# Kernel tuning notes

Measured on AMD Instinct MI355X. Metric: run time of the kernel, lower is better.

## Reference

```python
import jax, jax.numpy as jnp
import numpy as np

B, S, CIN, COUT, W, M, P = 32, 8192, 2, 1, 64, 16, 24


def setup_inputs() -> dict:
    key = jax.random.key(0)
    ks = jax.random.split(key, 12)

    def lin(k, o, i):
        return (jax.random.uniform(k, (o, i), jnp.float32) * 2 - 1) / np.float32(np.sqrt(i))

    scale = np.float32(1.0 / (W * W))  # SpectralConv1d init scale 1/(in*out)
    return {
        "x": jax.random.normal(ks[0], (B, S, CIN), jnp.float32),
        "fc0_w": lin(ks[1], W, CIN),
        "fc0_b": jnp.zeros((W,), jnp.float32),
        "conv_wr": jax.random.uniform(ks[2], (4, W, W, M), jnp.float32) * scale,
        "conv_wi": jax.random.uniform(ks[3], (4, W, W, M), jnp.float32) * scale,
        "pw_w": lin(ks[4], 4 * W, W).reshape(4, W, W),  # 1x1 conv weights (out,in)
        "pw_b": jnp.zeros((4, W), jnp.float32),
        "fc1_w": lin(ks[5], 128, W),
        "fc1_b": jnp.zeros((128,), jnp.float32),
        "fc2_w": lin(ks[6], COUT, 128),
        "ica_w": lin(ks[7], P, 128),
        "ica_b": jnp.zeros((P,), jnp.float32),
    }


def spectral_conv(h, wr, wi, n):
    # h: (B, W, S). Keep first M rfft modes, complex-multiply, inverse rfft.
    xf = jnp.fft.rfft(h, axis=-1)[..., :M]          # (B, W, M) complex
    w = wr + 1j * wi                                 # (W, W, M)
    of = jnp.einsum('bix,iox->box', xf, w)           # (B, W, M)
    of = jnp.pad(of, ((0, 0), (0, 0), (0, n // 2 + 1 - M)))
    return jnp.fft.irfft(of, n=n, axis=-1)


def reference(x, fc0_w, fc0_b, conv_wr, conv_wi, pw_w, pw_b, fc1_w, fc1_b, fc2_w, ica_w, ica_b):
    b, s, _ = x.shape
    h = x @ fc0_w.T + fc0_b                          # lift: (B, S, W)
    h = h.transpose(0, 2, 1)                         # (B, W, S)
    for l in range(4):
        x1 = spectral_conv(h, conv_wr[l], conv_wi[l], s)
        x2 = jnp.einsum('oi,bis->bos', pw_w[l], h) + pw_b[l][None, :, None]
        h = x1 + x2
        if l < 3:                                    # no relu after layer 3 (as in torch code)
            h = jax.nn.relu(h)
    h = h.transpose(0, 2, 1)                         # (B, S, W)
    h = h @ fc1_w.T + fc1_b                          # (B, S, 128)
    h_ = jax.nn.relu(h)
    # broadcast ICA decomposition: (B,S,1,128)*(1,1,COUT,128)
    components = h_[:, :, None, :] * fc2_w[None, None, :, :]
    tc = components @ ica_w.T + ica_b                # (B, S, COUT, P)
    out = tc.sum(-1)                                 # (B, S, COUT)
    return out, tc
```

## Files before the change

kernel.cpp:

```cpp
#include <hip/hip_runtime.h>
#include <math.h>

#define SB 8192
#define NB 32
#define WC 64
#define NM 16
#define NKC 32
#define NP 24
#define NSC 16
#define LP 132


__global__ __launch_bounds__(256) void k_table(float* __restrict__ T) {
    int s = blockIdx.x * 256 + threadIdx.x;
    float* row = T + (size_t)s * NKC;
    #pragma unroll
    for (int k = 0; k < NM; ++k) {
        int m = (k * s) & (SB - 1);
        double ang = (double)m * (6.283185307179586476925286766559 / (double)SB);
        row[2 * k]     = (float)cos(ang);
        row[2 * k + 1] = (float)sin(ang);
    }
}

__global__ __launch_bounds__(256) void k_prep(const float* __restrict__ ica_w,
                                              const float* __restrict__ fc2_w,
                                              float* __restrict__ icaT) {
    int tid = blockIdx.x * 256 + threadIdx.x;
    int c = tid / NP;
    int p = tid - c * NP;
    icaT[c * NP + p] = ica_w[p * 128 + c] * fc2_w[c];
}

__global__ __launch_bounds__(256) void k_prepw(const float* __restrict__ pw_w,
                                               float* __restrict__ pwT) {
    int tid = blockIdx.x * 256 + threadIdx.x;
    int l = tid >> 12, k = (tid >> 6) & 63, o = tid & 63;
    pwT[tid] = pw_w[(size_t)l * 4096 + o * 64 + k];
}

__global__ __launch_bounds__(256) void k_lift(const float* __restrict__ x,
                                              const float* __restrict__ fc0_w,
                                              const float* __restrict__ fc0_b,
                                              float* __restrict__ h) {
    int b = blockIdx.y;
    int s = blockIdx.x * 256 + threadIdx.x;
    float2 xv = ((const float2*)x)[(size_t)b * SB + s];
    #pragma unroll
    for (int w = 0; w < WC; ++w) {
        float v = fmaf(xv.x, fc0_w[2 * w], fmaf(xv.y, fc0_w[2 * w + 1], fc0_b[w]));
        h[((size_t)(b * WC + w)) * SB + s] = v;
    }
}

__global__ __launch_bounds__(256) void k_dft(const float* __restrict__ h,
                                             const float* __restrict__ T,
                                             float* __restrict__ xfp) {
    __shared__ float u[12800];
    int blk = blockIdx.x;
    int b  = blk >> 4;
    int sc = blk & (NSC - 1);
    int t  = threadIdx.x;
    int lane = t & 63;
    int wv = __builtin_amdgcn_readfirstlane(t >> 6);
    int g  = lane >> 3;
    int j8 = lane & 7;

    float acc[8][4];
    #pragma unroll
    for (int i = 0; i < 8; ++i)
        #pragma unroll
        for (int m = 0; m < 4; ++m) acc[i][m] = 0.f;

    int ch_s = t >> 2, part = t & 3;
    const float* hb = h + ((size_t)(b * WC + ch_s)) * SB;

    for (int st = 0; st < 4; ++st) {
        int s_base = sc * 512 + st * 128;

        const float* hrow = hb + s_base;
        #pragma unroll
        for (int r = 0; r < 8; ++r) {
            int so = (part + 4 * r) * 4;
            float4 v = *(const float4*)(hrow + so);
            u[(so + 0) * 68 + ch_s] = v.x;
            u[(so + 1) * 68 + ch_s] = v.y;
            u[(so + 2) * 68 + ch_s] = v.z;
            u[(so + 3) * 68 + ch_s] = v.w;
        }
        {
            const float4* tsrc = (const float4*)(T + (size_t)s_base * NKC);
            float4* tdst = (float4*)(u + 8704);
            #pragma unroll
            for (int r = 0; r < 4; ++r) tdst[t + r * 256] = tsrc[t + r * 256];
        }
        __syncthreads();

        #pragma unroll 4
        for (int ss = 0; ss < 32; ++ss) {
            int s = wv * 32 + ss;
            float4 tv = *(const float4*)&u[8704 + s * 32 + j8 * 4];
            float4 h0 = *(const float4*)&u[s * 68 + g * 8];
            float4 h1 = *(const float4*)&u[s * 68 + g * 8 + 4];
            float hh[8] = {h0.x, h0.y, h0.z, h0.w, h1.x, h1.y, h1.z, h1.w};
            #pragma unroll
            for (int i = 0; i < 8; ++i) {
                acc[i][0] = fmaf(hh[i], tv.x, acc[i][0]);
                acc[i][1] = fmaf(hh[i], tv.y, acc[i][1]);
                acc[i][2] = fmaf(hh[i], tv.z, acc[i][2]);
                acc[i][3] = fmaf(hh[i], tv.w, acc[i][3]);
            }
        }
        __syncthreads();
    }

    {
        float* slot = u + (wv * 64 + lane) * 33;
        #pragma unroll
        for (int i = 0; i < 8; ++i)
            #pragma unroll
            for (int m = 0; m < 4; ++m) slot[i * 4 + m] = acc[i][m];
    }
    __syncthreads();

    float* dst = xfp + ((size_t)(sc * NB + b)) * 2048;
    float res[8];
    #pragma unroll
    for (int e = 0; e < 8; ++e) {
        int idx = t * 8 + e;
        int ch = idx >> 5, mode = idx & 31;
        int g2 = ch >> 3, i2 = ch & 7;
        int q2 = mode >> 2, m2 = mode & 3;
        int lane2 = g2 * 8 + q2;
        int v2 = i2 * 4 + m2;
        res[e] = u[lane2 * 33 + v2] + u[(64 + lane2) * 33 + v2]
               + u[(128 + lane2) * 33 + v2] + u[(192 + lane2) * 33 + v2];
    }
    float4* d4 = (float4*)(dst + t * 8);
    d4[0] = make_float4(res[0], res[1], res[2], res[3]);
    d4[1] = make_float4(res[4], res[5], res[6], res[7]);
}

__global__ __launch_bounds__(256) void k_red(const float* __restrict__ xfp,
                                             float* __restrict__ xf, int nsc) {
    int idx = blockIdx.x * 256 + threadIdx.x;
    int b = idx >> 11;
    int r = idx & 2047;
    float s = 0.f;
    #pragma unroll 8
    for (int sc = 0; sc < nsc; ++sc)
        s += xfp[((size_t)(sc * NB + b)) * 2048 + r];
    xf[idx] = s;
}

__global__ __launch_bounds__(256) void k_mix(const float* __restrict__ xf,
                                             const float* __restrict__ wr,
                                             const float* __restrict__ wi,
                                             float* __restrict__ ofT) {
    int tid = blockIdx.x * 256 + threadIdx.x;
    int k = tid & 15;
    int o = (tid >> 4) & 63;
    int b = tid >> 10;
    float orr = 0.f, oii = 0.f;
    const float2* xfb = (const float2*)(xf + (size_t)b * WC * NKC);
    #pragma unroll 4
    for (int i = 0; i < WC; ++i) {
        float2 cs = xfb[i * NM + k];
        float wrv = wr[(i * WC + o) * NM + k];
        float wiv = wi[(i * WC + o) * NM + k];
        orr = fmaf(cs.x, wrv, fmaf(cs.y, wiv, orr));
        oii = fmaf(cs.x, wiv, fmaf(-cs.y, wrv, oii));
    }
    float alpha = (k == 0 ? 1.f : 2.f) / (float)SB;
    ofT[((size_t)b * NKC + 2 * k) * 64 + o]     = alpha * orr;
    ofT[((size_t)b * NKC + 2 * k + 1) * 64 + o] = -alpha * oii;
}

__global__ __launch_bounds__(256) void k_update(float* __restrict__ h,
                                                const float* __restrict__ T,
                                                const float* __restrict__ ofT,
                                                const float* __restrict__ pwT,
                                                const float* __restrict__ pwb,
                                                int relu, float* __restrict__ xfp,
                                                int dodft) {
    __shared__ float u[96 * LP];
    float (*hS)[LP] = (float(*)[LP])u;
    int t = threadIdx.x;
    int b = blockIdx.y;
    int s0 = blockIdx.x * 128;
    int lane_s = t & 63;
    int g4 = __builtin_amdgcn_readfirstlane((t >> 6) & 3);
    int ob = g4 * 16;

    {
        int ch = t >> 2, part = t & 3;
        const float* hrow = h + ((size_t)(b * WC + ch)) * SB + s0;
        #pragma unroll
        for (int r = 0; r < 8; ++r) {
            int so = (part + 4 * r) * 4;
            *(float4*)&hS[ch][so] = *(const float4*)(hrow + so);
        }
    }
    {
        int sl = t >> 1, jj0 = (t & 1) * 16;
        const float4* src = (const float4*)(T + (size_t)(s0 + sl) * NKC + jj0);
        float4 a = src[0], c4 = src[1], d = src[2], e = src[3];
        hS[64 + jj0 +  0][sl] = a.x;  hS[64 + jj0 +  1][sl] = a.y;
        hS[64 + jj0 +  2][sl] = a.z;  hS[64 + jj0 +  3][sl] = a.w;
        hS[64 + jj0 +  4][sl] = c4.x; hS[64 + jj0 +  5][sl] = c4.y;
        hS[64 + jj0 +  6][sl] = c4.z; hS[64 + jj0 +  7][sl] = c4.w;
        hS[64 + jj0 +  8][sl] = d.x;  hS[64 + jj0 +  9][sl] = d.y;
        hS[64 + jj0 + 10][sl] = d.z;  hS[64 + jj0 + 11][sl] = d.w;
        hS[64 + jj0 + 12][sl] = e.x;  hS[64 + jj0 + 13][sl] = e.y;
        hS[64 + jj0 + 14][sl] = e.z;  hS[64 + jj0 + 15][sl] = e.w;
    }
    __syncthreads();

    float acc0[16], acc1[16];
    #pragma unroll
    for (int o = 0; o < 16; ++o) { acc0[o] = pwb[ob + o]; acc1[o] = pwb[ob + o]; }

    const float* wbase0 = pwT + ob;
    const float* wbase1 = ofT + ((size_t)b * NKC) * 64 + ob;

    for (int kc = 0; kc < 8; ++kc) {
        #pragma unroll
        for (int uu = 0; uu < 8; ++uu) {
            int k = kc * 8 + uu;
            float h0 = hS[k][lane_s];
            float h1 = hS[k][64 + lane_s];
            const float* w = wbase0 + k * 64;
            #pragma unroll
            for (int o = 0; o < 16; ++o) {
                acc0[o] = fmaf(w[o], h0, acc0[o]);
                acc1[o] = fmaf(w[o], h1, acc1[o]);
            }
        }
    }
    for (int kc = 0; kc < 4; ++kc) {
        #pragma unroll
        for (int uu = 0; uu < 8; ++uu) {
            int j = kc * 8 + uu;
            float h0 = hS[64 + j][lane_s];
            float h1 = hS[64 + j][64 + lane_s];
            const float* w = wbase1 + j * 64;
            #pragma unroll
            for (int o = 0; o < 16; ++o) {
                acc0[o] = fmaf(w[o], h0, acc0[o]);
                acc1[o] = fmaf(w[o], h1, acc1[o]);
            }
        }
    }

    if (relu) {
        #pragma unroll
        for (int o = 0; o < 16; ++o) {
            acc0[o] = fmaxf(acc0[o], 0.f);
            acc1[o] = fmaxf(acc1[o], 0.f);
        }
    }

    float* hw0 = h + (size_t)b * WC * SB + s0 + lane_s;
    float* hw1 = hw0 + 64;
    #pragma unroll
    for (int o = 0; o < 16; ++o) {
        hw0[(size_t)(ob + o) * SB] = acc0[o];
        hw1[(size_t)(ob + o) * SB] = acc1[o];
    }

    if (!dodft) return;

    __syncthreads();
    #pragma unroll
    for (int o = 0; o < 16; ++o) {
        u[lane_s * 65 + ob + o]        = acc0[o];
        u[(64 + lane_s) * 65 + ob + o] = acc1[o];
    }
    __syncthreads();

    int lane = t & 63;
    int wv = __builtin_amdgcn_readfirstlane(t >> 6);
    int g  = lane >> 3;
    int j8 = lane & 7;

    float dacc[8][4];
    #pragma unroll
    for (int i = 0; i < 8; ++i)
        #pragma unroll
        for (int m = 0; m < 4; ++m) dacc[i][m] = 0.f;

    #pragma unroll 4
    for (int ss = 0; ss < 32; ++ss) {
        int s = wv * 32 + ss;
        float tv0 = u[64 * LP + (j8 * 4 + 0) * LP + s];
        float tv1 = u[64 * LP + (j8 * 4 + 1) * LP + s];
        float tv2 = u[64 * LP + (j8 * 4 + 2) * LP + s];
        float tv3 = u[64 * LP + (j8 * 4 + 3) * LP + s];
        float4 h0 = *(const float4*)&u[s * 65 + g * 8];
        float4 h1 = *(const float4*)&u[s * 65 + g * 8 + 4];
        float hh[8] = {h0.x, h0.y, h0.z, h0.w, h1.x, h1.y, h1.z, h1.w};
        #pragma unroll
        for (int i = 0; i < 8; ++i) {
            dacc[i][0] = fmaf(hh[i], tv0, dacc[i][0]);
            dacc[i][1] = fmaf(hh[i], tv1, dacc[i][1]);
            dacc[i][2] = fmaf(hh[i], tv2, dacc[i][2]);
            dacc[i][3] = fmaf(hh[i], tv3, dacc[i][3]);
        }
    }

    __syncthreads();
    {
        float* slot = u + (wv * 64 + lane) * 33;
        #pragma unroll
        for (int i = 0; i < 8; ++i)
            #pragma unroll
            for (int m = 0; m < 4; ++m) slot[i * 4 + m] = dacc[i][m];
    }
    __syncthreads();

    float* dst = xfp + ((size_t)(blockIdx.x * NB + b)) * 2048;
    float res[8];
    #pragma unroll
    for (int e = 0; e < 8; ++e) {
        int idx = t * 8 + e;
        int ch = idx >> 5, mode = idx & 31;
        int g2 = ch >> 3, i2 = ch & 7;
        int q2 = mode >> 2, m2 = mode & 3;
        int lane2 = g2 * 8 + q2;
        int v2 = i2 * 4 + m2;
        res[e] = u[lane2 * 33 + v2] + u[(64 + lane2) * 33 + v2]
               + u[(128 + lane2) * 33 + v2] + u[(192 + lane2) * 33 + v2];
    }
    float4* d4 = (float4*)(dst + t * 8);
    d4[0] = make_float4(res[0], res[1], res[2], res[3]);
    d4[1] = make_float4(res[4], res[5], res[6], res[7]);
}

__global__ __launch_bounds__(256) void k_final(const float* __restrict__ h,
                                               const float* __restrict__ fc1_w,
                                               const float* __restrict__ fc1_b,
                                               const float* __restrict__ icaT,
                                               const float* __restrict__ ica_b,
                                               float* __restrict__ out,
                                               float* __restrict__ tc) {
    __shared__ float u_lds[6400];
    float (*hS)[68] = (float(*)[68])u_lds;
    int t = threadIdx.x;
    int b = blockIdx.y;
    int s0 = blockIdx.x * 64;
    int lane_s = t & 63;
    int wv = __builtin_amdgcn_readfirstlane(t >> 6);
    int c0 = wv * 32;

    {
        int sl = t & 63, chg = t >> 6;
        const float* hb = h + (size_t)b * WC * SB + s0 + sl;
        #pragma unroll
        for (int cc = 0; cc < 16; ++cc) {
            int ch = chg * 16 + cc;
            hS[sl][ch] = hb[(size_t)ch * SB];
        }
    }
    __syncthreads();

    float acc[NP];
    #pragma unroll
    for (int p = 0; p < NP; ++p) acc[p] = 0.f;

    for (int cq = 0; cq < 8; ++cq) {
        int c = c0 + 4 * cq;
        float tv0 = fc1_b[c], tv1 = fc1_b[c + 1], tv2 = fc1_b[c + 2], tv3 = fc1_b[c + 3];
        const float* w0 = fc1_w + (size_t)c * WC;
        const float* w1 = w0 + WC;
        const float* w2 = w1 + WC;
        const float* w3 = w2 + WC;
        for (int ioct = 0; ioct < 8; ++ioct) {
            float4 xa = *(const float4*)&hS[lane_s][ioct * 8];
            float4 xb = *(const float4*)&hS[lane_s][ioct * 8 + 4];
            float xs[8] = {xa.x, xa.y, xa.z, xa.w, xb.x, xb.y, xb.z, xb.w};
            #pragma unroll
            for (int uu = 0; uu < 8; ++uu) {
                int i = ioct * 8 + uu;
                tv0 = fmaf(w0[i], xs[uu], tv0);
                tv1 = fmaf(w1[i], xs[uu], tv1);
                tv2 = fmaf(w2[i], xs[uu], tv2);
                tv3 = fmaf(w3[i], xs[uu], tv3);
            }
        }
        tv0 = fmaxf(tv0, 0.f); tv1 = fmaxf(tv1, 0.f);
        tv2 = fmaxf(tv2, 0.f); tv3 = fmaxf(tv3, 0.f);
        const float* e0 = icaT + (size_t)c * NP;
        const float* e1 = e0 + NP;
        const float* e2 = e1 + NP;
        const float* e3 = e2 + NP;
        #pragma unroll
        for (int p = 0; p < NP; ++p)
            acc[p] = fmaf(tv0, e0[p], fmaf(tv1, e1[p],
                     fmaf(tv2, e2[p], fmaf(tv3, e3[p], acc[p]))));
    }

    __syncthreads();
    {
        float* slot = u_lds + ((t >> 6) * 64 + lane_s) * 25;
        #pragma unroll
        for (int p = 0; p < NP; ++p) slot[p] = acc[p];
    }
    __syncthreads();

    float* tcb = tc + ((size_t)b * SB + s0) * NP;
    #pragma unroll
    for (int r = 0; r < 6; ++r) {
        int e = t + r * 256;
        int s = e / NP, p = e - s * NP;
        float v = u_lds[s * 25 + p] + u_lds[(64 + s) * 25 + p]
                + u_lds[(128 + s) * 25 + p] + u_lds[(192 + s) * 25 + p]
                + ica_b[p];
        tcb[e] = v;
        u_lds[s * 25 + p] = v;
    }
    __syncthreads();
    if (t < 64) {
        float osum = 0.f;
        #pragma unroll
        for (int p = 0; p < NP; ++p) osum += u_lds[t * 25 + p];
        out[(size_t)b * SB + s0 + t] = osum;
    }
}

extern "C" void kernel_launch(void* const* d_in, const int* in_sizes, int n_in,
                              void* d_out, int out_size, void* d_ws, size_t ws_size,
                              hipStream_t stream) {
    const float* x     = (const float*)d_in[0];
    const float* fc0_w = (const float*)d_in[1];
    const float* fc0_b = (const float*)d_in[2];
    const float* cwr   = (const float*)d_in[3];
    const float* cwi   = (const float*)d_in[4];
    const float* pw_w  = (const float*)d_in[5];
    const float* pw_b  = (const float*)d_in[6];
    const float* fc1_w = (const float*)d_in[7];
    const float* fc1_b = (const float*)d_in[8];
    const float* fc2_w = (const float*)d_in[9];
    const float* ica_w = (const float*)d_in[10];
    const float* ica_b = (const float*)d_in[11];

    float* out = (float*)d_out;
    float* tc  = out + (size_t)NB * SB;

    float* ws   = (float*)d_ws;
    float* h    = ws;
    float* T    = ws + 16777216;
    float* xf   = ws + 17039360;
    float* ofT  = ws + 17104896;
    float* icaT = ws + 17170432;
    float* pwT  = ws + 17173504;
    float* xfp  = tc;

    k_table<<<32, 256, 0, stream>>>(T);
    k_prep<<<12, 256, 0, stream>>>(ica_w, fc2_w, icaT);
    k_prepw<<<64, 256, 0, stream>>>(pw_w, pwT);
    k_lift<<<dim3(32, 32), 256, 0, stream>>>(x, fc0_w, fc0_b, h);

    for (int l = 0; l < 4; ++l) {
        if (l == 0) {
            k_dft<<<NB * NSC, 256, 0, stream>>>(h, T, xfp);
            k_red<<<256, 256, 0, stream>>>(xfp, xf, NSC);
        } else {
            k_red<<<256, 256, 0, stream>>>(xfp, xf, 64);
        }
        k_mix<<<128, 256, 0, stream>>>(xf, cwr + (size_t)l * WC * WC * NM,
                                       cwi + (size_t)l * WC * WC * NM, ofT);
        k_update<<<dim3(64, 32), 256, 0, stream>>>(h, T, ofT,
                                                   pwT + (size_t)l * 4096,
                                                   pw_b + (size_t)l * WC,
                                                   (l < 3) ? 1 : 0,
                                                   xfp, (l < 3) ? 1 : 0);
    }

    k_final<<<dim3(128, 32), 256, 0, stream>>>(h, fc1_w, fc1_b, icaT, ica_b, out, tc);
}
```

Measured before the change: 425.8 us.

## Fuse layer-0 truncated DFT into the lift kernel

The lift kernel now keeps each 128-sample tile of lifted activations in shared memory and computes the partial 16-mode DFT directly, writing per-chunk partials in the same 64-chunk format the later layers use. This removes the separate k_dft launch and its re-read of the full h tensor from global memory. The layer-0 reduction now sums 64 partials instead of 16, and the lift kernel carries more shared memory and register pressure.

```diff
diff --git a/kernel.cpp b/kernel.cpp
--- a/kernel.cpp
+++ b/kernel.cpp
@@ -7,7 +7,6 @@
 #define NM 16
 #define NKC 32
 #define NP 24
-#define NSC 16
 #define LP 132
 
 
@@ -42,88 +41,82 @@
 __global__ __launch_bounds__(256) void k_lift(const float* __restrict__ x,
                                               const float* __restrict__ fc0_w,
                                               const float* __restrict__ fc0_b,
-                                              float* __restrict__ h) {
+                                              float* __restrict__ h,
+                                              const float* __restrict__ T,
+                                              float* __restrict__ xfp) {
+    __shared__ float u[12544];
+    int t = threadIdx.x;
     int b = blockIdx.y;
-    int s = blockIdx.x * 256 + threadIdx.x;
-    float2 xv = ((const float2*)x)[(size_t)b * SB + s];
-    #pragma unroll
-    for (int w = 0; w < WC; ++w) {
-        float v = fmaf(xv.x, fc0_w[2 * w], fmaf(xv.y, fc0_w[2 * w + 1], fc0_b[w]));
-        h[((size_t)(b * WC + w)) * SB + s] = v;
-    }
-}
-
-__global__ __launch_bounds__(256) void k_dft(const float* __restrict__ h,
-                                             const float* __restrict__ T,
-                                             float* __restrict__ xfp) {
-    __shared__ float u[12800];
-    int blk = blockIdx.x;
-    int b  = blk >> 4;
-    int sc = blk & (NSC - 1);
-    int t  = threadIdx.x;
+    int s0 = blockIdx.x * 128;
+    int sl = t & 127, half = t >> 7;
+    int cb = half * 32;
+
+    float2 xv = ((const float2*)x)[(size_t)b * SB + s0 + sl];
+    float* hcol = h + (size_t)b * WC * SB + s0 + sl;
+    #pragma unroll
+    for (int c = 0; c < 32; ++c) {
+        int ch = cb + c;
+        float v = fmaf(xv.x, fc0_w[2 * ch], fmaf(xv.y, fc0_w[2 * ch + 1], fc0_b[ch]));
+        hcol[(size_t)ch * SB] = v;
+        u[sl * 65 + ch] = v;
+    }
+    {
+        int sl2 = t >> 1, jj0 = (t & 1) * 16;
+        const float4* src = (const float4*)(T + (size_t)(s0 + sl2) * NKC + jj0);
+        float4 a = src[0], c4 = src[1], d = src[2], e = src[3];
+        float* Tt = u + 8320;
+        Tt[(jj0 +  0) * LP + sl2] = a.x;  Tt[(jj0 +  1) * LP + sl2] = a.y;
+        Tt[(jj0 +  2) * LP + sl2] = a.z;  Tt[(jj0 +  3) * LP + sl2] = a.w;
+        Tt[(jj0 +  4) * LP + sl2] = c4.x; Tt[(jj0 +  5) * LP + sl2] = c4.y;
+        Tt[(jj0 +  6) * LP + sl2] = c4.z; Tt[(jj0 +  7) * LP + sl2] = c4.w;
+        Tt[(jj0 +  8) * LP + sl2] = d.x;  Tt[(jj0 +  9) * LP + sl2] = d.y;
+        Tt[(jj0 + 10) * LP + sl2] = d.z;  Tt[(jj0 + 11) * LP + sl2] = d.w;
+        Tt[(jj0 + 12) * LP + sl2] = e.x;  Tt[(jj0 + 13) * LP + sl2] = e.y;
+        Tt[(jj0 + 14) * LP + sl2] = e.z;  Tt[(jj0 + 15) * LP + sl2] = e.w;
+    }
+    __syncthreads();
+
     int lane = t & 63;
     int wv = __builtin_amdgcn_readfirstlane(t >> 6);
     int g  = lane >> 3;
     int j8 = lane & 7;
 
-    float acc[8][4];
+    float dacc[8][4];
     #pragma unroll
     for (int i = 0; i < 8; ++i)
         #pragma unroll
-        for (int m = 0; m < 4; ++m) acc[i][m] = 0.f;
-
-    int ch_s = t >> 2, part = t & 3;
-    const float* hb = h + ((size_t)(b * WC + ch_s)) * SB;
-
-    for (int st = 0; st < 4; ++st) {
-        int s_base = sc * 512 + st * 128;
-
-        const float* hrow = hb + s_base;
-        #pragma unroll
-        for (int r = 0; r < 8; ++r) {
-            int so = (part + 4 * r) * 4;
-            float4 v = *(const float4*)(hrow + so);
-            u[(so + 0) * 68 + ch_s] = v.x;
-            u[(so + 1) * 68 + ch_s] = v.y;
-            u[(so + 2) * 68 + ch_s] = v.z;
-            u[(so + 3) * 68 + ch_s] = v.w;
-        }
-        {
-            const float4* tsrc = (const float4*)(T + (size_t)s_base * NKC);
-            float4* tdst = (float4*)(u + 8704);
-            #pragma unroll
-            for (int r = 0; r < 4; ++r) tdst[t + r * 256] = tsrc[t + r * 256];
-        }
-        __syncthreads();
-
-        #pragma unroll 4
-        for (int ss = 0; ss < 32; ++ss) {
-            int s = wv * 32 + ss;
-            float4 tv = *(const float4*)&u[8704 + s * 32 + j8 * 4];
-            float4 h0 = *(const float4*)&u[s * 68 + g * 8];
-            float4 h1 = *(const float4*)&u[s * 68 + g * 8 + 4];
-            float hh[8] = {h0.x, h0.y, h0.z, h0.w, h1.x, h1.y, h1.z, h1.w};
-            #pragma unroll
-            for (int i = 0; i < 8; ++i) {
-                acc[i][0] = fmaf(hh[i], tv.x, acc[i][0]);
-                acc[i][1] = fmaf(hh[i], tv.y, acc[i][1]);
-                acc[i][2] = fmaf(hh[i], tv.z, acc[i][2]);
-                acc[i][3] = fmaf(hh[i], tv.w, acc[i][3]);
-            }
-        }
-        __syncthreads();
-    }
-
+        for (int m = 0; m < 4; ++m) dacc[i][m] = 0.f;
+
+    #pragma unroll 4
+    for (int ss = 0; ss < 32; ++ss) {
+        int s = wv * 32 + ss;
+        float tv0 = u[8320 + (j8 * 4 + 0) * LP + s];
+        float tv1 = u[8320 + (j8 * 4 + 1) * LP + s];
+        float tv2 = u[8320 + (j8 * 4 + 2) * LP + s];
+        float tv3 = u[8320 + (j8 * 4 + 3) * LP + s];
+        float4 h0 = *(const float4*)&u[s * 65 + g * 8];
+        float4 h1 = *(const float4*)&u[s * 65 + g * 8 + 4];
+        float hh[8] = {h0.x, h0.y, h0.z, h0.w, h1.x, h1.y, h1.z, h1.w};
+        #pragma unroll
+        for (int i = 0; i < 8; ++i) {
+            dacc[i][0] = fmaf(hh[i], tv0, dacc[i][0]);
+            dacc[i][1] = fmaf(hh[i], tv1, dacc[i][1]);
+            dacc[i][2] = fmaf(hh[i], tv2, dacc[i][2]);
+            dacc[i][3] = fmaf(hh[i], tv3, dacc[i][3]);
+        }
+    }
+
+    __syncthreads();
     {
         float* slot = u + (wv * 64 + lane) * 33;
         #pragma unroll
         for (int i = 0; i < 8; ++i)
             #pragma unroll
-            for (int m = 0; m < 4; ++m) slot[i * 4 + m] = acc[i][m];
-    }
-    __syncthreads();
-
-    float* dst = xfp + ((size_t)(sc * NB + b)) * 2048;
+            for (int m = 0; m < 4; ++m) slot[i * 4 + m] = dacc[i][m];
+    }
+    __syncthreads();
+
+    float* dst = xfp + ((size_t)(blockIdx.x * NB + b)) * 2048;
     float res[8];
     #pragma unroll
     for (int e = 0; e < 8; ++e) {
@@ -458,15 +451,10 @@
     k_table<<<32, 256, 0, stream>>>(T);
     k_prep<<<12, 256, 0, stream>>>(ica_w, fc2_w, icaT);
     k_prepw<<<64, 256, 0, stream>>>(pw_w, pwT);
-    k_lift<<<dim3(32, 32), 256, 0, stream>>>(x, fc0_w, fc0_b, h);
+    k_lift<<<dim3(64, 32), 256, 0, stream>>>(x, fc0_w, fc0_b, h, T, xfp);
 
     for (int l = 0; l < 4; ++l) {
-        if (l == 0) {
-            k_dft<<<NB * NSC, 256, 0, stream>>>(h, T, xfp);
-            k_red<<<256, 256, 0, stream>>>(xfp, xf, NSC);
-        } else {
-            k_red<<<256, 256, 0, stream>>>(xfp, xf, 64);
-        }
+        k_red<<<256, 256, 0, stream>>>(xfp, xf, 64);
         k_mix<<<128, 256, 0, stream>>>(xf, cwr + (size_t)l * WC * WC * NM,
                                        cwi + (size_t)l * WC * WC * NM, ofT);
         k_update<<<dim3(64, 32), 256, 0, stream>>>(h, T, ofT,
```

Result: faster. 409.6 us (-3.8%).
